# Kernel tuning notes

Measured on AMD Instinct MI355X. Metric: run time of the kernel, lower is better.

The kernel has to match this reference:

```python
import jax, jax.numpy as jnp
import numpy as np

B, T, E, H = 4, 2048, 1024, 16
HD = E // H  # head_size = 64


def setup_inputs() -> dict:
    key = jax.random.key(0)
    ks = jax.random.split(key, 6)
    s = 1.0 / np.sqrt(E)
    x = jax.random.normal(ks[0], (B, T, E), dtype=jnp.float32)
    # per-head Q/K/V projection weights, stacked over heads: [H, E, HD]
    Wq = jax.random.uniform(ks[1], (H, E, HD), minval=-s, maxval=s, dtype=jnp.float32)
    Wk = jax.random.uniform(ks[2], (H, E, HD), minval=-s, maxval=s, dtype=jnp.float32)
    Wv = jax.random.uniform(ks[3], (H, E, HD), minval=-s, maxval=s, dtype=jnp.float32)
    Wo = jax.random.uniform(ks[4], (E, E), minval=-s, maxval=s, dtype=jnp.float32)
    bo = jax.random.uniform(ks[5], (E,), minval=-s, maxval=s, dtype=jnp.float32)
    return {"x": x, "Wq": Wq, "Wk": Wk, "Wv": Wv, "Wo": Wo, "bo": bo}


def reference(x, Wq, Wk, Wv, Wo, bo):
    # x: [B,T,E] -> q,k,v: [B,H,T,HD]
    q = jnp.einsum('bte,hed->bhtd', x, Wq)
    k = jnp.einsum('bte,hed->bhtd', x, Wk)
    v = jnp.einsum('bte,hed->bhtd', x, Wv)
    scale = HD ** -0.5
    scores = jnp.einsum('bhtd,bhsd->bhts', q, k) * scale  # [B,H,T,T]
    causal = jnp.tril(jnp.ones((T, T), dtype=bool))
    scores = jnp.where(causal, scores, -jnp.inf)
    wei = jax.nn.softmax(scores, axis=-1)  # dropout is identity in eval
    out = jnp.einsum('bhts,bhsd->bhtd', wei, v)  # [B,H,T,HD]
    out = out.transpose(0, 2, 1, 3).reshape(B, T, E)  # concat heads
    return out @ Wo.T + bo
```

## Files before the change

### kernel.cpp

```cpp
#include <hip/hip_runtime.h>
#include <hip/hip_bf16.h>

#define B_  4
#define T_  2048
#define E_  1024
#define H_  16
#define HD_ 64

typedef __hip_bfloat16 bf16;
typedef unsigned short u16;
using bf16x8 = __attribute__((ext_vector_type(8))) short;
using f32x4  = __attribute__((ext_vector_type(4))) float;

__device__ __forceinline__ float b2f(bf16 x) { return __bfloat162float(x); }
__device__ __forceinline__ bf16  f2b(float x) { return __float2bfloat16(x); }
__device__ __forceinline__ u16 f2b_bits(float x) {
    union { bf16 h; u16 u; } cv; cv.h = __float2bfloat16(x); return cv.u;
}
__device__ __forceinline__ float bits2f(u16 u) {
    union { float f; unsigned int i; } cv; cv.i = ((unsigned int)u) << 16; return cv.f;
}

__device__ __forceinline__ void gld_lds16(const void* g, void* lds) {
    void* gv = (void*)g;
    __builtin_amdgcn_global_load_lds(
        (__attribute__((address_space(1))) void*)gv,
        (__attribute__((address_space(3))) void*)lds, 16, 0, 0);
}

__global__ __launch_bounds__(256) void cast_bf16(
    const float* __restrict__ src, bf16* __restrict__ dst)
{
    size_t i = ((size_t)blockIdx.x * 256 + threadIdx.x) * 8;
    float4 a = *(const float4*)(src + i);
    float4 b = *(const float4*)(src + i + 4);
    u16 o[8] = { f2b_bits(a.x), f2b_bits(a.y), f2b_bits(a.z), f2b_bits(a.w),
                 f2b_bits(b.x), f2b_bits(b.y), f2b_bits(b.z), f2b_bits(b.w) };
    *(uint4*)(dst + i) = *(const uint4*)o;
}

__global__ __launch_bounds__(256) void cast_w_t(
    const float* __restrict__ Wq, const float* __restrict__ Wk,
    const float* __restrict__ Wv, bf16* __restrict__ Wt)
{
    const float* W = (blockIdx.z == 0) ? Wq : (blockIdx.z == 1) ? Wk : Wv;
    const float scl = (blockIdx.z == 0) ? 0.125f : 1.0f;
    bf16* dst = Wt + (size_t)blockIdx.z * (H_ * HD_ * E_);
    const int h = blockIdx.y, k0 = blockIdx.x * 64;
    __shared__ float Ws[64][65];
    const int tid = threadIdx.x;
    {
        int kk = tid >> 2, d0 = (tid & 3) * 16;
        const float* p = W + ((size_t)h * E_ + k0 + kk) * HD_ + d0;
        #pragma unroll
        for (int i = 0; i < 4; i++) {
            float4 f = *(const float4*)(p + i * 4);
            Ws[kk][d0 + i * 4 + 0] = f.x; Ws[kk][d0 + i * 4 + 1] = f.y;
            Ws[kk][d0 + i * 4 + 2] = f.z; Ws[kk][d0 + i * 4 + 3] = f.w;
        }
    }
    __syncthreads();
    {
        int d = tid >> 2, kc = (tid & 3) * 16;
        u16 o[16];
        #pragma unroll
        for (int j = 0; j < 16; j++) o[j] = f2b_bits(Ws[kc + j][d] * scl);
        bf16* p = dst + ((size_t)h * HD_ + d) * E_ + k0 + kc;
        *(uint4*)(p)     = *(const uint4*)&o[0];
        *(uint4*)(p + 8) = *(const uint4*)&o[8];
    }
}

__global__ __launch_bounds__(256) void qkv_mfma(
    const bf16* __restrict__ xb, const bf16* __restrict__ Wt,
    bf16* __restrict__ q, bf16* __restrict__ k, bf16* __restrict__ v)
{
    const int n0 = blockIdx.x * 128;
    const int m0 = blockIdx.y * 128;
    const int z  = n0 >> 10;
    bf16* out = (z == 0) ? q : (z == 1) ? k : v;
    const int tid = threadIdx.x, lane = tid & 63, w = tid >> 6;
    const int wm = w >> 1, wn = w & 1;
    const int quad = lane >> 4, l15 = lane & 15;

    __shared__ __align__(16) u16 smem[2 * 128 * 64];
    u16* As = smem;
    u16* Bs = smem + 128 * 64;

    f32x4 acc[4][4];
    #pragma unroll
    for (int i = 0; i < 4; i++)
        #pragma unroll
        for (int j = 0; j < 4; j++) acc[i][j] = f32x4{0.f, 0.f, 0.f, 0.f};

    const int srow = lane >> 3;
    const int scol = ((lane & 7) ^ srow) * 8;
    const bf16* agp = xb + (size_t)(m0 + w * 32 + srow) * E_ + scol;
    const bf16* bgp = Wt + (size_t)(n0 + w * 32 + srow) * E_ + scol;
    u16* alds = As + (w * 32) * 64;
    u16* blds = Bs + (w * 32) * 64;
    const int rsw = l15 & 7;

    for (int k0 = 0; k0 < E_; k0 += 64) {
        __syncthreads();
        #pragma unroll
        for (int i = 0; i < 4; i++) {
            gld_lds16(agp + (size_t)(i * 8) * E_ + k0, alds + i * 8 * 64);
            gld_lds16(bgp + (size_t)(i * 8) * E_ + k0, blds + i * 8 * 64);
        }
        __syncthreads();

        #pragma unroll
        for (int ks = 0; ks < 2; ks++) {
            const int csw = ((ks * 4 + quad) ^ rsw) * 8;
            bf16x8 af[4];
            #pragma unroll
            for (int i = 0; i < 4; i++)
                af[i] = *(const bf16x8*)&As[(wm * 64 + i * 16 + l15) * 64 + csw];
            #pragma unroll
            for (int j = 0; j < 4; j++) {
                bf16x8 bfr = *(const bf16x8*)&Bs[(wn * 64 + j * 16 + l15) * 64 + csw];
                #pragma unroll
                for (int i = 0; i < 4; i++)
                    acc[i][j] = __builtin_amdgcn_mfma_f32_16x16x32_bf16(af[i], bfr, acc[i][j], 0, 0, 0);
            }
        }
    }

    if (z != 2) {
        const int h = ((n0 & 1023) >> 6) + wn;
        #pragma unroll
        for (int i = 0; i < 4; i++)
            #pragma unroll
            for (int r = 0; r < 4; r++) {
                int m = m0 + wm * 64 + i * 16 + quad * 4 + r;
                int bb2 = m >> 11, t = m & (T_ - 1);
                bf16* orow = out + ((size_t)(bb2 * H_ + h) * T_ + t) * HD_;
                #pragma unroll
                for (int j = 0; j < 4; j++)
                    orow[j * 16 + l15] = f2b(acc[i][j][r]);
            }
    } else {
        u16 (*Vt)[136] = (u16(*)[136])smem;
        const int bb2 = m0 >> 11, t0 = m0 & (T_ - 1);
        #pragma unroll
        for (int half = 0; half < 2; half++) {
            __syncthreads();
            if (wn == half) {
                #pragma unroll
                for (int j = 0; j < 4; j++)
                    #pragma unroll
                    for (int i = 0; i < 4; i++) {
                        ushort4 pk;
                        pk.x = f2b_bits(acc[i][j][0]);
                        pk.y = f2b_bits(acc[i][j][1]);
                        pk.z = f2b_bits(acc[i][j][2]);
                        pk.w = f2b_bits(acc[i][j][3]);
                        *(ushort4*)&Vt[j * 16 + l15][wm * 64 + i * 16 + quad * 4] = pk;
                    }
            }
            __syncthreads();
            {
                int dd = tid >> 2, tt = (tid & 3) * 32;
                int h = ((n0 & 1023) >> 6) + half;
                bf16* dst = out + ((size_t)(bb2 * H_ + h) * HD_ + dd) * T_ + t0 + tt;
                #pragma unroll
                for (int u = 0; u < 4; u++)
                    *(uint4*)(dst + u * 8) = *(const uint4*)&Vt[dd][tt + u * 8];
            }
        }
    }
}

__global__ __launch_bounds__(256) void flash_attn(
    const bf16* __restrict__ q, const bf16* __restrict__ k,
    const bf16* __restrict__ vt, bf16* __restrict__ att)
{
    const int bh = blockIdx.x & 63;
    const int qt = 31 - (blockIdx.x >> 6);
    const int q0 = qt * 64;
    const int hh = bh & 15, bb = bh >> 4;
    const int tid = threadIdx.x, lane = tid & 63, wave = tid >> 6;
    const int quad = lane >> 4, l15 = lane & 15;

    __shared__ __align__(16) u16 Ks[2][64 * 64];
    __shared__ __align__(16) u16 Vs[2][64 * 64];
    __shared__ __align__(16) u16 P2[4][1024];

    const size_t baseK = (size_t)bh * T_ * HD_;
    const bf16* vbase = vt + (size_t)bh * (size_t)HD_ * T_;

    const int qg = q0 + wave * 16 + l15;
    const bf16* qrow = q + baseK + (size_t)qg * HD_;
    bf16x8 qfrag[2];
    qfrag[0] = *(const bf16x8*)(qrow + quad * 8);
    qfrag[1] = *(const bf16x8*)(qrow + 32 + quad * 8);

    bf16x8 onesf;
    #pragma unroll
    for (int i = 0; i < 8; i++) onesf[i] = (short)0x3F80;

    f32x4 o[4];
    #pragma unroll
    for (int dt = 0; dt < 4; dt++) o[dt] = f32x4{0.f, 0.f, 0.f, 0.f};
    f32x4 lacc = f32x4{0.f, 0.f, 0.f, 0.f};

    const int q_in = wave * 16 + l15;

    const int srow = lane >> 3;
    const int scol = ((lane & 7) ^ srow) * 8;
    const bf16* kgp = k + baseK + (size_t)(wave * 16 + srow) * HD_ + scol;
    const bf16* vgp = vbase + (size_t)(wave * 16 + srow) * T_ + scol;
    u16* pw = P2[wave];
    const int rsw = l15 & 7;

    #define STAGE(b, s0) do {                                                 \
        gld_lds16(kgp + (size_t)(s0) * HD_,       &Ks[b][wave * 1024]);       \
        gld_lds16(kgp + (size_t)((s0) + 8) * HD_, &Ks[b][wave * 1024 + 512]); \
        gld_lds16(vgp + (s0),                     &Vs[b][wave * 1024]);       \
        gld_lds16(vgp + (s0) + 8 * T_,            &Vs[b][wave * 1024 + 512]); \
    } while (0)

    STAGE(0, 0);
    int cur = 0;

    for (int st = 0; st <= qt; st++) {
        if (st < qt) {
            STAGE(cur ^ 1, (st + 1) * 64);
            asm volatile("s_waitcnt vmcnt(4)" ::: "memory");
        } else {
            asm volatile("s_waitcnt vmcnt(0)" ::: "memory");
        }
        __builtin_amdgcn_s_barrier();
        __builtin_amdgcn_sched_barrier(0);

        f32x4 s[4];
        __builtin_amdgcn_s_setprio(1);
        #pragma unroll
        for (int ct = 0; ct < 4; ct++) {
            f32x4 a = f32x4{0.f, 0.f, 0.f, 0.f};
            #pragma unroll
            for (int ks = 0; ks < 2; ks++) {
                const int csw = ((ks * 4 + quad) ^ rsw) * 8;
                bf16x8 kfrag = *(const bf16x8*)&Ks[cur][(ct * 16 + l15) * 64 + csw];
                a = __builtin_amdgcn_mfma_f32_16x16x32_bf16(kfrag, qfrag[ks], a, 0, 0, 0);
            }
            s[ct] = a;
        }
        __builtin_amdgcn_s_setprio(0);

        if (st == qt) {
            #pragma unroll
            for (int ct = 0; ct < 4; ct++) {
                int sbase = ct * 16 + quad * 4;
                #pragma unroll
                for (int r = 0; r < 4; r++)
                    if (sbase + r > q_in) s[ct][r] = -1e30f;
            }
        }

        #pragma unroll
        for (int ct = 0; ct < 4; ct++) {
            ushort4 pk;
            pk.x = f2b_bits(__builtin_amdgcn_exp2f(__fmaf_rn(s[ct][0], 1.4426950408889634f, -11.541560327111707f)));
            pk.y = f2b_bits(__builtin_amdgcn_exp2f(__fmaf_rn(s[ct][1], 1.4426950408889634f, -11.541560327111707f)));
            pk.z = f2b_bits(__builtin_amdgcn_exp2f(__fmaf_rn(s[ct][2], 1.4426950408889634f, -11.541560327111707f)));
            pk.w = f2b_bits(__builtin_amdgcn_exp2f(__fmaf_rn(s[ct][3], 1.4426950408889634f, -11.541560327111707f)));
            *(ushort4*)&pw[(ct >> 1) * 512
                           + (((((ct & 1) << 1) | (quad >> 1)) * 16 + l15) * 8)
                           + (quad & 1) * 4] = pk;
        }

        __builtin_amdgcn_s_setprio(1);
        #pragma unroll
        for (int ks = 0; ks < 2; ks++) {
            bf16x8 pfrag = *(const bf16x8*)&pw[ks * 512 + (quad * 16 + l15) * 8];
            lacc = __builtin_amdgcn_mfma_f32_16x16x32_bf16(onesf, pfrag, lacc, 0, 0, 0);
            #pragma unroll
            for (int dt = 0; dt < 4; dt++) {
                const int csw = ((ks * 4 + quad) ^ rsw) * 8;
                bf16x8 vfrag = *(const bf16x8*)&Vs[cur][(dt * 16 + l15) * 64 + csw];
                o[dt] = __builtin_amdgcn_mfma_f32_16x16x32_bf16(vfrag, pfrag, o[dt], 0, 0, 0);
            }
        }
        __builtin_amdgcn_s_setprio(0);

        __builtin_amdgcn_sched_barrier(0);
        __builtin_amdgcn_s_barrier();
        cur ^= 1;
    }
    #undef STAGE

    float inv = 1.0f / lacc[0];
    bf16* orow = att + ((size_t)(bb * T_ + qg) * H_ + hh) * HD_;
    #pragma unroll
    for (int dt = 0; dt < 4; dt++) {
        ushort4 pk;
        pk.x = f2b_bits(o[dt][0] * inv);
        pk.y = f2b_bits(o[dt][1] * inv);
        pk.z = f2b_bits(o[dt][2] * inv);
        pk.w = f2b_bits(o[dt][3] * inv);
        *(ushort4*)(orow + dt * 16 + quad * 4) = pk;
    }
}

__global__ __launch_bounds__(256, 3) void out_proj_mfma(
    const bf16* __restrict__ att, const bf16* __restrict__ Wob,
    const float* __restrict__ bo, float* __restrict__ out)
{
    const int m0 = blockIdx.x * 128, n0 = blockIdx.y * 128;
    const int tid = threadIdx.x, lane = tid & 63, w = tid >> 6;
    const int wm = w >> 1, wn = w & 1;
    const int quad = lane >> 4, l15 = lane & 15;

    __shared__ __align__(16) u16 As[128 * 32];
    __shared__ __align__(16) u16 Bs[128 * 32];

    f32x4 acc[4][4];
    #pragma unroll
    for (int i = 0; i < 4; i++)
        #pragma unroll
        for (int j = 0; j < 4; j++) acc[i][j] = f32x4{0.f, 0.f, 0.f, 0.f};

    const int srow = lane >> 2;
    const int scol = ((lane & 3) ^ (srow & 3)) * 8;
    const bf16* agp = att + (size_t)(m0 + w * 32 + srow) * E_ + scol;
    const bf16* bgp = Wob + (size_t)(n0 + w * 32 + srow) * E_ + scol;
    u16* alds = As + (w * 32) * 32;
    u16* blds = Bs + (w * 32) * 32;
    const int rsw3 = l15 & 3;

    for (int k0 = 0; k0 < E_; k0 += 32) {
        __syncthreads();
        #pragma unroll
        for (int i = 0; i < 2; i++) {
            gld_lds16(agp + (size_t)(i * 16) * E_ + k0, alds + i * 16 * 32);
            gld_lds16(bgp + (size_t)(i * 16) * E_ + k0, blds + i * 16 * 32);
        }
        __syncthreads();

        const int csw = (quad ^ rsw3) * 8;
        bf16x8 af[4];
        #pragma unroll
        for (int i = 0; i < 4; i++)
            af[i] = *(const bf16x8*)&As[(wm * 64 + i * 16 + l15) * 32 + csw];
        #pragma unroll
        for (int j = 0; j < 4; j++) {
            bf16x8 bfr = *(const bf16x8*)&Bs[(wn * 64 + j * 16 + l15) * 32 + csw];
            #pragma unroll
            for (int i = 0; i < 4; i++)
                acc[i][j] = __builtin_amdgcn_mfma_f32_16x16x32_bf16(af[i], bfr, acc[i][j], 0, 0, 0);
        }
    }

    float bias[4];
    #pragma unroll
    for (int j = 0; j < 4; j++) bias[j] = bo[n0 + wn * 64 + j * 16 + l15];
    #pragma unroll
    for (int i = 0; i < 4; i++)
        #pragma unroll
        for (int r = 0; r < 4; r++) {
            int m = m0 + wm * 64 + i * 16 + quad * 4 + r;
            float* orow = out + (size_t)m * E_ + n0 + wn * 64;
            #pragma unroll
            for (int j = 0; j < 4; j++)
                orow[j * 16 + l15] = acc[i][j][r] + bias[j];
        }
}

extern "C" void kernel_launch(void* const* d_in, const int* in_sizes, int n_in,
                              void* d_out, int out_size, void* d_ws, size_t ws_size,
                              hipStream_t stream)
{
    const float* x  = (const float*)d_in[0];
    const float* Wq = (const float*)d_in[1];
    const float* Wk = (const float*)d_in[2];
    const float* Wv = (const float*)d_in[3];
    const float* Wo = (const float*)d_in[4];
    const float* bo = (const float*)d_in[5];
    float* out = (float*)d_out;

    const size_t elts = (size_t)B_ * H_ * T_ * HD_;
    bf16* att = (bf16*)d_ws;
    bf16* Wt  = att;
    bf16* q   = att + elts;
    bf16* Wob = q;
    bf16* k   = q + elts;
    bf16* v   = k + elts;
    bf16* xb  = (bf16*)d_out;

    cast_bf16<<<dim3((unsigned)(elts / 2048)), 256, 0, stream>>>(x, xb);
    cast_w_t<<<dim3(E_ / 64, H_, 3), 256, 0, stream>>>(Wq, Wk, Wv, Wt);

    qkv_mfma<<<dim3(3 * E_ / 128, (B_ * T_) / 128), 256, 0, stream>>>(xb, Wt, q, k, v);

    flash_attn<<<dim3((T_ / 64) * B_ * H_), 256, 0, stream>>>(q, k, v, att);

    cast_bf16<<<dim3((E_ * E_) / 2048), 256, 0, stream>>>(Wo, Wob);

    out_proj_mfma<<<dim3((B_ * T_) / 128, E_ / 128), 256, 0, stream>>>(att, Wob, bo, out);
}
```

Measured before the change: 245.7 us.

## Double-buffer LDS staging in QKV and output projection GEMMs

Converts the QKV projection and output projection GEMM main loops to double-buffered LDS, issuing the next K-tile's global-to-LDS loads before computing on the current tile. Partial vmcnt waits and raw s_barrier replace the two __syncthreads per iteration, and MFMA sections are wrapped in s_setprio to favour compute waves. This is meant to hide global load latency behind MFMA work. In exchange it doubles LDS use per block: 64KB in qkv, which may cut occupancy. It also depends on exact vmcnt counts matching the issued loads.

```diff
diff --git a/kernel.cpp b/kernel.cpp
--- a/kernel.cpp
+++ b/kernel.cpp
@@ -83,9 +83,7 @@
     const int wm = w >> 1, wn = w & 1;
     const int quad = lane >> 4, l15 = lane & 15;
 
-    __shared__ __align__(16) u16 smem[2 * 128 * 64];
-    u16* As = smem;
-    u16* Bs = smem + 128 * 64;
+    __shared__ __align__(16) u16 smem[2 * 2 * 128 * 64];
 
     f32x4 acc[4][4];
     #pragma unroll
@@ -97,19 +95,34 @@
     const int scol = ((lane & 7) ^ srow) * 8;
     const bf16* agp = xb + (size_t)(m0 + w * 32 + srow) * E_ + scol;
     const bf16* bgp = Wt + (size_t)(n0 + w * 32 + srow) * E_ + scol;
-    u16* alds = As + (w * 32) * 64;
-    u16* blds = Bs + (w * 32) * 64;
     const int rsw = l15 & 7;
 
+    #define QSTAGE(b, kk) do {                                                \
+        u16* a_ = smem + (b) * 16384 + (w * 32) * 64;                         \
+        u16* b_ = smem + (b) * 16384 + 8192 + (w * 32) * 64;                  \
+        _Pragma("unroll")                                                     \
+        for (int i_ = 0; i_ < 4; i_++) {                                      \
+            gld_lds16(agp + (size_t)(i_ * 8) * E_ + (kk), a_ + i_ * 8 * 64);  \
+            gld_lds16(bgp + (size_t)(i_ * 8) * E_ + (kk), b_ + i_ * 8 * 64);  \
+        }                                                                     \
+    } while (0)
+
+    QSTAGE(0, 0);
+    int cur = 0;
+
     for (int k0 = 0; k0 < E_; k0 += 64) {
-        __syncthreads();
-        #pragma unroll
-        for (int i = 0; i < 4; i++) {
-            gld_lds16(agp + (size_t)(i * 8) * E_ + k0, alds + i * 8 * 64);
-            gld_lds16(bgp + (size_t)(i * 8) * E_ + k0, blds + i * 8 * 64);
-        }
-        __syncthreads();
-
+        if (k0 + 64 < E_) {
+            QSTAGE(cur ^ 1, k0 + 64);
+            asm volatile("s_waitcnt vmcnt(8)" ::: "memory");
+        } else {
+            asm volatile("s_waitcnt vmcnt(0)" ::: "memory");
+        }
+        __builtin_amdgcn_s_barrier();
+        __builtin_amdgcn_sched_barrier(0);
+
+        const u16* As = smem + cur * 16384;
+        const u16* Bs = As + 8192;
+        __builtin_amdgcn_s_setprio(1);
         #pragma unroll
         for (int ks = 0; ks < 2; ks++) {
             const int csw = ((ks * 4 + quad) ^ rsw) * 8;
@@ -125,7 +138,13 @@
                     acc[i][j] = __builtin_amdgcn_mfma_f32_16x16x32_bf16(af[i], bfr, acc[i][j], 0, 0, 0);
             }
         }
-    }
+        __builtin_amdgcn_s_setprio(0);
+
+        __builtin_amdgcn_sched_barrier(0);
+        __builtin_amdgcn_s_barrier();
+        cur ^= 1;
+    }
+    #undef QSTAGE
 
     if (z != 2) {
         const int h = ((n0 & 1023) >> 6) + wn;
@@ -313,8 +332,7 @@
     const int wm = w >> 1, wn = w & 1;
     const int quad = lane >> 4, l15 = lane & 15;
 
-    __shared__ __align__(16) u16 As[128 * 32];
-    __shared__ __align__(16) u16 Bs[128 * 32];
+    __shared__ __align__(16) u16 smem[2 * 2 * 128 * 32];
 
     f32x4 acc[4][4];
     #pragma unroll
@@ -326,20 +344,35 @@
     const int scol = ((lane & 3) ^ (srow & 3)) * 8;
     const bf16* agp = att + (size_t)(m0 + w * 32 + srow) * E_ + scol;
     const bf16* bgp = Wob + (size_t)(n0 + w * 32 + srow) * E_ + scol;
-    u16* alds = As + (w * 32) * 32;
-    u16* blds = Bs + (w * 32) * 32;
     const int rsw3 = l15 & 3;
 
+    #define OSTAGE(b, kk) do {                                                \
+        u16* a_ = smem + (b) * 8192 + (w * 32) * 32;                          \
+        u16* b_ = smem + (b) * 8192 + 4096 + (w * 32) * 32;                   \
+        _Pragma("unroll")                                                     \
+        for (int i_ = 0; i_ < 2; i_++) {                                      \
+            gld_lds16(agp + (size_t)(i_ * 16) * E_ + (kk), a_ + i_ * 16 * 32);\
+            gld_lds16(bgp + (size_t)(i_ * 16) * E_ + (kk), b_ + i_ * 16 * 32);\
+        }                                                                     \
+    } while (0)
+
+    OSTAGE(0, 0);
+    int cur = 0;
+
     for (int k0 = 0; k0 < E_; k0 += 32) {
-        __syncthreads();
-        #pragma unroll
-        for (int i = 0; i < 2; i++) {
-            gld_lds16(agp + (size_t)(i * 16) * E_ + k0, alds + i * 16 * 32);
-            gld_lds16(bgp + (size_t)(i * 16) * E_ + k0, blds + i * 16 * 32);
-        }
-        __syncthreads();
-
+        if (k0 + 32 < E_) {
+            OSTAGE(cur ^ 1, k0 + 32);
+            asm volatile("s_waitcnt vmcnt(4)" ::: "memory");
+        } else {
+            asm volatile("s_waitcnt vmcnt(0)" ::: "memory");
+        }
+        __builtin_amdgcn_s_barrier();
+        __builtin_amdgcn_sched_barrier(0);
+
+        const u16* As = smem + cur * 8192;
+        const u16* Bs = As + 4096;
         const int csw = (quad ^ rsw3) * 8;
+        __builtin_amdgcn_s_setprio(1);
         bf16x8 af[4];
         #pragma unroll
         for (int i = 0; i < 4; i++)
@@ -351,7 +384,13 @@
             for (int i = 0; i < 4; i++)
                 acc[i][j] = __builtin_amdgcn_mfma_f32_16x16x32_bf16(af[i], bfr, acc[i][j], 0, 0, 0);
         }
-    }
+        __builtin_amdgcn_s_setprio(0);
+
+        __builtin_amdgcn_sched_barrier(0);
+        __builtin_amdgcn_s_barrier();
+        cur ^= 1;
+    }
+    #undef OSTAGE
 
     float bias[4];
     #pragma unroll
```

Result: faster. 232.7 us (-5.3%).
